# Optimization experiments

Hardware: AMD Instinct MI355X
Metric: run time of the kernel (lower is better)

Reference implementation:

```python
import jax, jax.numpy as jnp
import numpy as np

D_MODEL = 2048
N_HEADS = 16
KV_HEADS = 4
HEAD_DIM = D_MODEL // N_HEADS  # 128
GROUPS = N_HEADS // KV_HEADS   # 4
CLIP_QKV = 8.0
EPS = 1e-5
MAX_POS = 2048
ROPE_THETA = 10000.0


def _make_rope(max_pos, dim, theta):
    inv_freq = 1.0 / (theta ** (np.arange(0, dim, 2, dtype=np.float32) / dim))
    t = np.arange(max_pos, dtype=np.float32)
    freqs = np.outer(t, inv_freq)                      # [max_pos, dim/2]
    emb = np.concatenate([freqs, freqs], axis=-1)      # [max_pos, dim]
    return jnp.asarray(np.sin(emb)), jnp.asarray(np.cos(emb))


def setup_inputs() -> dict:
    key = jax.random.key(0)
    ks = jax.random.split(key, 6)
    B, S = 2, 2048
    hidden_states = jax.random.normal(ks[0], (B, S, D_MODEL), dtype=jnp.float32)
    attention_mask = jnp.ones((B, S), dtype=jnp.int32)
    position_ids = jnp.broadcast_to(jnp.arange(S, dtype=jnp.int32)[None, :], (B, S))
    init_std = 0.02
    qkv_out = D_MODEL + 2 * KV_HEADS * HEAD_DIM
    wqkv = jax.random.normal(ks[1], (D_MODEL, qkv_out), dtype=jnp.float32) * init_std
    w_out = jax.random.normal(ks[2], (D_MODEL, D_MODEL), dtype=jnp.float32) * init_std
    norm1_w = jnp.ones((D_MODEL,), dtype=jnp.float32)
    norm2_w = jnp.ones((D_MODEL,), dtype=jnp.float32)
    rope_sin, rope_cos = _make_rope(MAX_POS, HEAD_DIM, ROPE_THETA)
    return {
        'hidden_states': hidden_states,
        'attention_mask': attention_mask,
        'position_ids': position_ids,
        'wqkv': wqkv,
        'w_out': w_out,
        'norm1_w': norm1_w,
        'norm2_w': norm2_w,
        'rope_sin': rope_sin,
        'rope_cos': rope_cos,
    }


def _rmsnorm(x, w, eps=EPS):
    var = jnp.mean(jnp.square(x), axis=-1, keepdims=True)
    return (x * jax.lax.rsqrt(var + eps)) * w


def _rotate_half(x):
    h = x.shape[-1] // 2
    return jnp.concatenate([-x[..., h:], x[..., :h]], axis=-1)


def reference(hidden_states, attention_mask, position_ids, wqkv, w_out, norm1_w, norm2_w, rope_sin, rope_cos):
    B, S, _ = hidden_states.shape
    residual = hidden_states
    # pre-norm
    x = _rmsnorm(hidden_states, norm1_w)
    # fused QKV projection + clip
    qkv = jnp.clip(x @ wqkv, -CLIP_QKV, CLIP_QKV)
    q = qkv[..., :D_MODEL].reshape(B, S, N_HEADS, HEAD_DIM)
    kv_sz = KV_HEADS * HEAD_DIM
    k = qkv[..., D_MODEL:D_MODEL + kv_sz].reshape(B, S, KV_HEADS, HEAD_DIM)
    v = qkv[..., D_MODEL + kv_sz:].reshape(B, S, KV_HEADS, HEAD_DIM)
    # rotary embedding (bshd layout)
    sin = rope_sin[position_ids][:, :, None, :]  # [B,S,1,hd]
    cos = rope_cos[position_ids][:, :, None, :]
    q = q * cos + _rotate_half(q) * sin
    k = k * cos + _rotate_half(k) * sin
    # GQA head repeat
    k = jnp.repeat(k, GROUPS, axis=2)  # [B,S,H,hd]
    v = jnp.repeat(v, GROUPS, axis=2)
    # attention
    scale = 1.0 / jnp.sqrt(jnp.float32(HEAD_DIM))
    scores = jnp.einsum('bqhd,bkhd->bhqk', q, k) * scale
    causal = jnp.tril(jnp.ones((S, S), dtype=bool))
    mask = causal[None, None, :, :] & (attention_mask[:, None, None, :] > 0)
    scores = jnp.where(mask, scores, jnp.finfo(scores.dtype).min)
    probs = jax.nn.softmax(scores, axis=-1)
    attn = jnp.einsum('bhqk,bkhd->bqhd', probs, v).reshape(B, S, D_MODEL)
    attn = attn @ w_out
    # residual add (resid dropout deterministic -> identity) + post-norm
    hidden = residual + attn
    residual_out = hidden
    post = _rmsnorm(hidden, norm2_w)
    return residual_out, post
```

## Files before the change

kernel.cpp:

```cpp
#include <hip/hip_runtime.h>
#include <cstdint>
#include <cstddef>

#define D_MODEL 2048
#define SEQ     2048
#define NB      2
#define ROWS    4096
#define QKV_N   3072
#define NH      16
#define NKV     4
#define HD      128
#define EPSV    1e-5f
#define QPRE    (0.08838834764831845f * 1.4426950408889634f)

typedef unsigned short ushort_t;
typedef __attribute__((ext_vector_type(8))) short  short8;
typedef __attribute__((ext_vector_type(4))) short  short4v;
typedef __attribute__((ext_vector_type(4))) float  floatx4;

__device__ __forceinline__ ushort_t f2b(float f) {
    unsigned u = __float_as_uint(f);
    u += 0x7fffu + ((u >> 16) & 1u);
    return (ushort_t)(u >> 16);
}
__device__ __forceinline__ float b2f(ushort_t u) {
    return __uint_as_float(((unsigned)u) << 16);
}

__device__ __forceinline__ unsigned pkbf(float lo, float hi) {
    unsigned u0 = __float_as_uint(lo) + 0x8000u;
    unsigned u1 = __float_as_uint(hi) + 0x8000u;
    return __builtin_amdgcn_perm(u1, u0, 0x07060302u);
}

#if __has_builtin(__builtin_amdgcn_mfma_f32_16x16x16bf16_1k)
#define HAVE_1K 1
#endif

__device__ __forceinline__ floatx4 pv_mfma(short4v a, short4v b, floatx4 c) {
#ifdef HAVE_1K
    return __builtin_amdgcn_mfma_f32_16x16x16bf16_1k(a, b, c, 0, 0, 0);
#else
    short8 a8 = {a[0], a[1], a[2], a[3], 0, 0, 0, 0};
    short8 b8 = {b[0], b[1], b[2], b[3], 0, 0, 0, 0};
    return __builtin_amdgcn_mfma_f32_16x16x32_bf16(a8, b8, c, 0, 0, 0);
#endif
}

#define GLD_LDS16(gp, lp) __builtin_amdgcn_global_load_lds( \
    (const __attribute__((address_space(1))) void*)(gp),   \
    (__attribute__((address_space(3))) void*)(lp), 16, 0, 0)

__global__ __launch_bounds__(256) void k_rmsnorm_bf16(
        const float* __restrict__ x, const float* __restrict__ w,
        ushort_t* __restrict__ out) {
    int row = blockIdx.x, t = threadIdx.x;
    const float4* xr = (const float4*)(x + (size_t)row * D_MODEL);
    float4 a = xr[t], b = xr[t + 256];
    float ss = a.x*a.x + a.y*a.y + a.z*a.z + a.w*a.w
             + b.x*b.x + b.y*b.y + b.z*b.z + b.w*b.w;
    for (int m = 1; m < 64; m <<= 1) ss += __shfl_xor(ss, m);
    __shared__ float sred[4];
    if ((t & 63) == 0) sred[t >> 6] = ss;
    __syncthreads();
    float r = rsqrtf((sred[0] + sred[1] + sred[2] + sred[3]) * (1.0f / D_MODEL) + EPSV);
    const float4* wr = (const float4*)w;
    float4 wa = wr[t], wb = wr[t + 256];
    ushort4 pa, pb;
    pa.x = f2b(a.x * r * wa.x); pa.y = f2b(a.y * r * wa.y);
    pa.z = f2b(a.z * r * wa.z); pa.w = f2b(a.w * r * wa.w);
    pb.x = f2b(b.x * r * wb.x); pb.y = f2b(b.y * r * wb.y);
    pb.z = f2b(b.z * r * wb.z); pb.w = f2b(b.w * r * wb.w);
    ushort4* o = (ushort4*)(out + (size_t)row * D_MODEL);
    o[t] = pa; o[t + 256] = pb;
}

__global__ __launch_bounds__(256) void k_rmsnorm_f32(
        const float* __restrict__ x, const float* __restrict__ w,
        float* __restrict__ out) {
    int row = blockIdx.x, t = threadIdx.x;
    const float4* xr = (const float4*)(x + (size_t)row * D_MODEL);
    float4 a = xr[t], b = xr[t + 256];
    float ss = a.x*a.x + a.y*a.y + a.z*a.z + a.w*a.w
             + b.x*b.x + b.y*b.y + b.z*b.z + b.w*b.w;
    for (int m = 1; m < 64; m <<= 1) ss += __shfl_xor(ss, m);
    __shared__ float sred[4];
    if ((t & 63) == 0) sred[t >> 6] = ss;
    __syncthreads();
    float r = rsqrtf((sred[0] + sred[1] + sred[2] + sred[3]) * (1.0f / D_MODEL) + EPSV);
    const float4* wr = (const float4*)w;
    float4 wa = wr[t], wb = wr[t + 256];
    float4 oa, ob;
    oa.x = a.x * r * wa.x; oa.y = a.y * r * wa.y; oa.z = a.z * r * wa.z; oa.w = a.w * r * wa.w;
    ob.x = b.x * r * wb.x; ob.y = b.y * r * wb.y; ob.z = b.z * r * wb.z; ob.w = b.w * r * wb.w;
    float4* o = (float4*)(out + (size_t)row * D_MODEL);
    o[t] = oa; o[t + 256] = ob;
}

__global__ __launch_bounds__(256) void k_transpose_cvt(
        const float* __restrict__ in, ushort_t* __restrict__ out, int R, int C) {
    __shared__ float tile[32][33];
    int bc = blockIdx.x * 32, br = blockIdx.y * 32;
    int t = threadIdx.x, lr = t >> 5, lc = t & 31;
    for (int i = 0; i < 4; i++)
        tile[lr + i * 8][lc] = in[(size_t)(br + lr + i * 8) * C + bc + lc];
    __syncthreads();
    for (int i = 0; i < 4; i++)
        out[(size_t)(bc + lr + i * 8) * R + br + lc] = f2b(tile[lc][lr + i * 8]);
}

template <int MODE>
__global__ __launch_bounds__(256) void k_gemm(
        const ushort_t* __restrict__ A, const ushort_t* __restrict__ Bt,
        void* __restrict__ Cout, const float* __restrict__ resid,
        int M, int N, int K) {
    __shared__ __align__(16) ushort_t sA[128 * 32];
    __shared__ __align__(16) ushort_t sB[128 * 32];
    int bm = blockIdx.y * 128, bn = blockIdx.x * 128;
    int t = threadIdx.x;
    int wv = t >> 6, lane = t & 63;
    int wm = (wv >> 1) * 64, wn = (wv & 1) * 64;
    int q4 = lane >> 4, n16 = lane & 15;

    int srow = lane >> 2, scol = (lane & 3) * 8;
    const ushort_t* gA0 = A  + (size_t)(bm + wv * 32 + srow) * K + scol;
    const ushort_t* gA1 = gA0 + (size_t)16 * K;
    const ushort_t* gB0 = Bt + (size_t)(bn + wv * 32 + srow) * K + scol;
    const ushort_t* gB1 = gB0 + (size_t)16 * K;
    ushort_t* lA0 = sA + wv * 1024;
    ushort_t* lA1 = lA0 + 512;
    ushort_t* lB0 = sB + wv * 1024;
    ushort_t* lB1 = lB0 + 512;

    floatx4 zero4 = {0.0f, 0.0f, 0.0f, 0.0f};
    floatx4 acc[4][4];
    for (int i = 0; i < 4; i++)
        for (int j = 0; j < 4; j++) acc[i][j] = zero4;

    for (int k0 = 0; k0 < K; k0 += 32) {
        GLD_LDS16(gA0 + k0, lA0);
        GLD_LDS16(gA1 + k0, lA1);
        GLD_LDS16(gB0 + k0, lB0);
        GLD_LDS16(gB1 + k0, lB1);
        __syncthreads();
        short8 af[4], bfr[4];
        for (int i = 0; i < 4; i++) af[i]  = *(const short8*)&sA[(wm + i * 16 + n16) * 32 + q4 * 8];
        for (int j = 0; j < 4; j++) bfr[j] = *(const short8*)&sB[(wn + j * 16 + n16) * 32 + q4 * 8];
        for (int i = 0; i < 4; i++)
            for (int j = 0; j < 4; j++)
                acc[i][j] = __builtin_amdgcn_mfma_f32_16x16x32_bf16(af[i], bfr[j], acc[i][j], 0, 0, 0);
        __syncthreads();
    }

    for (int i = 0; i < 4; i++) {
        int rbase = bm + wm + i * 16 + q4 * 4;
        for (int j = 0; j < 4; j++) {
            int col = bn + wn + j * 16 + n16;
            if (MODE == 0) {
                ushort_t* C = (ushort_t*)Cout;
                for (int r = 0; r < 4; r++) {
                    float v = acc[i][j][r];
                    v = fminf(fmaxf(v, -8.0f), 8.0f);
                    C[(size_t)(rbase + r) * N + col] = f2b(v);
                }
            } else {
                float* C = (float*)Cout;
                for (int r = 0; r < 4; r++) {
                    float v = acc[i][j][r] + resid[(size_t)(rbase + r) * N + col];
                    C[(size_t)(rbase + r) * N + col] = v;
                }
            }
        }
    }
}

__global__ __launch_bounds__(256) void k_rope(
        const ushort_t* __restrict__ qkv, const int* __restrict__ pos_ids,
        const float* __restrict__ rsin, const float* __restrict__ rcos,
        ushort_t* __restrict__ qout, ushort_t* __restrict__ kout) {
    int wid  = blockIdx.x * 4 + (threadIdx.x >> 6);
    int lane = threadIdx.x & 63;
    int row = wid / 20, slot = wid - row * 20;
    int b = row >> 11, s = row & 2047;
    int pos = pos_ids[row];
    int col0 = (slot < 16) ? slot * HD : D_MODEL + (slot - 16) * HD;
    const ushort_t* src = qkv + (size_t)row * QKV_N + col0;
    float xl = b2f(src[lane]);
    float xh = b2f(src[lane + 64]);
    const float* cp = rcos + (size_t)pos * HD;
    const float* sp = rsin + (size_t)pos * HD;
    float cl = cp[lane], sl = sp[lane];
    float ch = cp[lane + 64], sh = sp[lane + 64];
    float mul = (slot < 16) ? QPRE : 1.0f;
    float ol = (xl * cl - xh * sl) * mul;
    float oh = (xh * ch + xl * sh) * mul;
    if (slot < 16) {
        size_t dst = ((size_t)(b * NH + slot) * SEQ + s) * HD;
        qout[dst + lane] = f2b(ol); qout[dst + lane + 64] = f2b(oh);
    } else {
        size_t dst = ((size_t)(b * NKV + (slot - 16)) * SEQ + s) * HD;
        kout[dst + lane] = f2b(ol); kout[dst + lane + 64] = f2b(oh);
    }
}

__global__ __launch_bounds__(256) void k_vtrans(
        const ushort_t* __restrict__ qkv, ushort_t* __restrict__ vt) {
    __shared__ ushort_t tile[32][33];
    int bh = blockIdx.z;
    int b = bh >> 2, h = bh & 3;
    int s0 = blockIdx.x * 32, d0 = blockIdx.y * 32;
    int t = threadIdx.x, lr = t >> 5, lc = t & 31;
    int col0 = D_MODEL + NKV * HD + h * HD;
    for (int i = 0; i < 4; i++)
        tile[lr + i * 8][lc] =
            qkv[((size_t)b * SEQ + s0 + lr + i * 8) * QKV_N + col0 + d0 + lc];
    __syncthreads();
    for (int i = 0; i < 4; i++)
        vt[((size_t)bh * HD + d0 + lr + i * 8) * SEQ + s0 + lc] = tile[lc][lr + i * 8];
}

__global__ __launch_bounds__(256, 4) void k_attn(
        const ushort_t* __restrict__ Q, const ushort_t* __restrict__ Kr,
        const ushort_t* __restrict__ Vt, const int* __restrict__ amask,
        ushort_t* __restrict__ O) {
    int bidx = blockIdx.x;
    int qt = (SEQ / 64 - 1) - (bidx >> 5);
    int bh = bidx & 31, h = bh & 15, b = bh >> 4;
    int wave = threadIdx.x >> 6, lane = threadIdx.x & 63;
    int q4 = lane >> 4, n16 = lane & 15;

    __shared__ __align__(16) ushort_t sK[64 * 128];
    __shared__ __align__(16) ushort_t sV[128 * 64];

    const ushort_t* Qh = Q  + (size_t)bh * SEQ * HD;
    const ushort_t* Kh = Kr + (size_t)(b * NKV + (h >> 2)) * SEQ * HD;
    const ushort_t* Vh = Vt + (size_t)(b * NKV + (h >> 2)) * HD * SEQ;
    const int* am = amask + b * SEQ;

    int q0 = qt * 64 + wave * 16;
    int qcol = q0 + n16;

    short8 qf[4];
    for (int kk = 0; kk < 4; kk++)
        qf[kk] = *(const short8*)(Qh + (size_t)qcol * HD + kk * 32 + q4 * 8);

    floatx4 zero4 = {0.0f, 0.0f, 0.0f, 0.0f};
    floatx4 o_acc[8];
    for (int dt = 0; dt < 8; dt++) o_acc[dt] = zero4;
    float m_i = -INFINITY, l_i = 0.0f;

    int krow_l = (lane >> 4);
    int kc_l   = lane & 15;
    int vrow_l = (lane >> 3);
    int vc_l   = lane & 7;

    int kv_iters = qt + 1;
    for (int it = 0; it < kv_iters; it++) {
        int kv0 = it * 64;
        __syncthreads();
        #pragma unroll
        for (int t = 0; t < 4; t++) {
            int krow = wave * 16 + t * 4 + krow_l;
            int kc   = kc_l ^ (krow & 7);
            GLD_LDS16(Kh + (size_t)(kv0 + krow) * HD + kc * 8,
                      sK + (wave * 16 + t * 4) * 128);
            int vrow = wave * 32 + t * 8 + vrow_l;
            int vc   = vc_l ^ (vrow & 7);
            GLD_LDS16(Vh + (size_t)vrow * SEQ + kv0 + vc * 8,
                      sV + (wave * 32 + t * 8) * 64);
        }
        __syncthreads();

        bool tail = (kv0 + 63 > q0);
        floatx4 st[4];
        for (int jj = 0; jj < 4; jj++) st[jj] = zero4;
        for (int jj = 0; jj < 4; jj++) {
            int krow = jj * 16 + n16;
            int sw = krow & 7;
            const ushort_t* kb = sK + krow * 128;
            for (int kk = 0; kk < 4; kk++) {
                short8 kf = *(const short8*)(kb + ((kk * 4 + q4) ^ sw) * 8);
                st[jj] = __builtin_amdgcn_mfma_f32_16x16x32_bf16(kf, qf[kk], st[jj], 0, 0, 0);
            }
        }
        for (int jj = 0; jj < 4; jj++) {
            int kvb = kv0 + jj * 16 + q4 * 4;
            int4 am4 = *(const int4*)(am + kvb);
            int amr[4] = {am4.x, am4.y, am4.z, am4.w};
            if (tail) {
                for (int r = 0; r < 4; r++)
                    st[jj][r] = (amr[r] > 0 && kvb + r <= qcol) ? st[jj][r] : -1e30f;
            } else {
                for (int r = 0; r < 4; r++)
                    st[jj][r] = (amr[r] > 0) ? st[jj][r] : -1e30f;
            }
        }
        float mx = st[0][0];
        for (int jj = 0; jj < 4; jj++)
            for (int r = 0; r < 4; r++) mx = fmaxf(mx, st[jj][r]);
        mx = fmaxf(mx, __shfl_xor(mx, 16));
        mx = fmaxf(mx, __shfl_xor(mx, 32));
        float mnew = fmaxf(m_i, mx);
        float al = exp2f(m_i - mnew);
        m_i = mnew;
        float rs = 0.0f;
        for (int jj = 0; jj < 4; jj++)
            for (int r = 0; r < 4; r++) {
                float p = exp2f(st[jj][r] - mnew);
                st[jj][r] = p;
                rs += p;
            }
        rs += __shfl_xor(rs, 16);
        rs += __shfl_xor(rs, 32);
        l_i = l_i * al + rs;
        for (int dt = 0; dt < 8; dt++)
            o_acc[dt] *= al;
        for (int jj = 0; jj < 4; jj++) {
            union { unsigned u[2]; short4v s; } uu;
            uu.u[0] = pkbf(st[jj][0], st[jj][1]);
            uu.u[1] = pkbf(st[jj][2], st[jj][3]);
            short4v pfr = uu.s;
            int ch = jj * 2 + (q4 >> 1), hh = q4 & 1;
            for (int dt = 0; dt < 8; dt++) {
                int vrow = dt * 16 + n16;
                short4v vf = *(const short4v*)(sV + vrow * 64 + ((ch ^ (vrow & 7)) * 8) + hh * 4);
                o_acc[dt] = pv_mfma(vf, pfr, o_acc[dt]);
            }
        }
    }
    float inv = 1.0f / l_i;
    ushort_t* orow = O + ((size_t)(b * SEQ) + qcol) * D_MODEL + h * HD + q4 * 4;
    for (int dt = 0; dt < 8; dt++) {
        uint2 pk;
        pk.x = pkbf(o_acc[dt][0] * inv, o_acc[dt][1] * inv);
        pk.y = pkbf(o_acc[dt][2] * inv, o_acc[dt][3] * inv);
        *(uint2*)(orow + dt * 16) = pk;
    }
}

extern "C" void kernel_launch(void* const* d_in, const int* in_sizes, int n_in,
                              void* d_out, int out_size, void* d_ws, size_t ws_size,
                              hipStream_t stream) {
    const float* hidden = (const float*)d_in[0];
    const int*   amask  = (const int*)d_in[1];
    const int*   pos    = (const int*)d_in[2];
    const float* wqkv   = (const float*)d_in[3];
    const float* wout   = (const float*)d_in[4];
    const float* n1w    = (const float*)d_in[5];
    const float* n2w    = (const float*)d_in[6];
    const float* rsin   = (const float*)d_in[7];
    const float* rcos   = (const float*)d_in[8];
    float* out0 = (float*)d_out;
    float* out1 = out0 + (size_t)ROWS * D_MODEL;

    char* ws = (char*)d_ws;
    ushort_t* x_bf    = (ushort_t*)ws;  ws += (size_t)ROWS * D_MODEL * 2;
    ushort_t* wqkv_t  = (ushort_t*)ws;  ws += (size_t)QKV_N * D_MODEL * 2;
    ushort_t* wout_t  = (ushort_t*)ws;  ws += (size_t)D_MODEL * D_MODEL * 2;
    ushort_t* qkv     = (ushort_t*)ws;  ws += (size_t)ROWS * QKV_N * 2;
    ushort_t* qrot    = (ushort_t*)ws;  ws += (size_t)NB * NH * SEQ * HD * 2;
    ushort_t* krot    = (ushort_t*)ws;  ws += (size_t)NB * NKV * SEQ * HD * 2;
    ushort_t* vt      = (ushort_t*)ws;  ws += (size_t)NB * NKV * HD * SEQ * 2;
    ushort_t* attn    = (ushort_t*)ws;  ws += (size_t)ROWS * D_MODEL * 2;

    k_rmsnorm_bf16<<<ROWS, 256, 0, stream>>>(hidden, n1w, x_bf);
    k_transpose_cvt<<<dim3(QKV_N / 32, D_MODEL / 32), 256, 0, stream>>>(wqkv, wqkv_t, D_MODEL, QKV_N);
    k_transpose_cvt<<<dim3(D_MODEL / 32, D_MODEL / 32), 256, 0, stream>>>(wout, wout_t, D_MODEL, D_MODEL);
    k_gemm<0><<<dim3(QKV_N / 128, ROWS / 128), 256, 0, stream>>>(x_bf, wqkv_t, qkv, nullptr, ROWS, QKV_N, D_MODEL);
    k_rope<<<ROWS * 20 / 4, 256, 0, stream>>>(qkv, pos, rsin, rcos, qrot, krot);
    k_vtrans<<<dim3(SEQ / 32, HD / 32, NB * NKV), 256, 0, stream>>>(qkv, vt);
    k_attn<<<(SEQ / 64) * 32, 256, 0, stream>>>(qrot, krot, vt, amask, attn);
    k_gemm<1><<<dim3(D_MODEL / 128, ROWS / 128), 256, 0, stream>>>(attn, wout_t, out0, hidden, ROWS, D_MODEL, D_MODEL);
    k_rmsnorm_f32<<<ROWS, 256, 0, stream>>>(out0, n2w, out1);
}
```

Before: 392.1 us.

## Double-buffer K/V tiles in attention and skip rescale when max grows little

Splits the K/V shared-memory staging into two buffers so the next tile's global-to-LDS load is issued while the current tile is computed, with one barrier per iteration in place of two. It also adds a lazy online-softmax rescale: the accumulator and running sum are rescaled only when the new row max exceeds the old one by more than 8 (log2 domain). Occupancy is lowered to 2 blocks per CU because LDS per block doubles. The lazy rescale lets exp2 arguments reach up to 2^8, which relies on fp32 headroom and bf16 packing of probabilities above 1.

```diff
diff --git a/kernel.cpp b/kernel.cpp
--- a/kernel.cpp
+++ b/kernel.cpp
@@ -219,7 +219,7 @@
         vt[((size_t)bh * HD + d0 + lr + i * 8) * SEQ + s0 + lc] = tile[lc][lr + i * 8];
 }
 
-__global__ __launch_bounds__(256, 4) void k_attn(
+__global__ __launch_bounds__(256, 2) void k_attn(
         const ushort_t* __restrict__ Q, const ushort_t* __restrict__ Kr,
         const ushort_t* __restrict__ Vt, const int* __restrict__ amask,
         ushort_t* __restrict__ O) {
@@ -229,8 +229,8 @@
     int wave = threadIdx.x >> 6, lane = threadIdx.x & 63;
     int q4 = lane >> 4, n16 = lane & 15;
 
-    __shared__ __align__(16) ushort_t sK[64 * 128];
-    __shared__ __align__(16) ushort_t sV[128 * 64];
+    __shared__ __align__(16) ushort_t sK[2][64 * 128];
+    __shared__ __align__(16) ushort_t sV[2][128 * 64];
 
     const ushort_t* Qh = Q  + (size_t)bh * SEQ * HD;
     const ushort_t* Kh = Kr + (size_t)(b * NKV + (h >> 2)) * SEQ * HD;
@@ -254,22 +254,35 @@
     int vrow_l = (lane >> 3);
     int vc_l   = lane & 7;
 
-    int kv_iters = qt + 1;
-    for (int it = 0; it < kv_iters; it++) {
-        int kv0 = it * 64;
-        __syncthreads();
+    auto stage_kv = [&](int buf, int kv0) {
         #pragma unroll
         for (int t = 0; t < 4; t++) {
             int krow = wave * 16 + t * 4 + krow_l;
             int kc   = kc_l ^ (krow & 7);
             GLD_LDS16(Kh + (size_t)(kv0 + krow) * HD + kc * 8,
-                      sK + (wave * 16 + t * 4) * 128);
+                      &sK[buf][(wave * 16 + t * 4) * 128]);
             int vrow = wave * 32 + t * 8 + vrow_l;
             int vc   = vc_l ^ (vrow & 7);
             GLD_LDS16(Vh + (size_t)vrow * SEQ + kv0 + vc * 8,
-                      sV + (wave * 32 + t * 8) * 64);
-        }
-        __syncthreads();
+                      &sV[buf][(wave * 32 + t * 8) * 64]);
+        }
+    };
+
+    int kv_iters = qt + 1;
+
+    stage_kv(0, 0);
+    asm volatile("s_waitcnt vmcnt(0)" ::: "memory");
+    __builtin_amdgcn_s_barrier();
+    __builtin_amdgcn_sched_barrier(0);
+
+    for (int it = 0; it < kv_iters; it++) {
+        int cur = it & 1;
+        int kv0 = it * 64;
+        if (it + 1 < kv_iters)
+            stage_kv(cur ^ 1, kv0 + 64);
+
+        const ushort_t* sKc = sK[cur];
+        const ushort_t* sVc = sV[cur];
 
         bool tail = (kv0 + 63 > q0);
         floatx4 st[4];
@@ -277,7 +290,7 @@
         for (int jj = 0; jj < 4; jj++) {
             int krow = jj * 16 + n16;
             int sw = krow & 7;
-            const ushort_t* kb = sK + krow * 128;
+            const ushort_t* kb = sKc + krow * 128;
             for (int kk = 0; kk < 4; kk++) {
                 short8 kf = *(const short8*)(kb + ((kk * 4 + q4) ^ sw) * 8);
                 st[jj] = __builtin_amdgcn_mfma_f32_16x16x32_bf16(kf, qf[kk], st[jj], 0, 0, 0);
@@ -300,21 +313,24 @@
             for (int r = 0; r < 4; r++) mx = fmaxf(mx, st[jj][r]);
         mx = fmaxf(mx, __shfl_xor(mx, 16));
         mx = fmaxf(mx, __shfl_xor(mx, 32));
-        float mnew = fmaxf(m_i, mx);
-        float al = exp2f(m_i - mnew);
-        m_i = mnew;
+        if (!__all(mx - m_i <= 8.0f)) {
+            float mnew = fmaxf(m_i, mx);
+            float al = exp2f(m_i - mnew);
+            m_i = mnew;
+            l_i *= al;
+            for (int dt = 0; dt < 8; dt++)
+                o_acc[dt] *= al;
+        }
         float rs = 0.0f;
         for (int jj = 0; jj < 4; jj++)
             for (int r = 0; r < 4; r++) {
-                float p = exp2f(st[jj][r] - mnew);
+                float p = exp2f(st[jj][r] - m_i);
                 st[jj][r] = p;
                 rs += p;
             }
         rs += __shfl_xor(rs, 16);
         rs += __shfl_xor(rs, 32);
-        l_i = l_i * al + rs;
-        for (int dt = 0; dt < 8; dt++)
-            o_acc[dt] *= al;
+        l_i += rs;
         for (int jj = 0; jj < 4; jj++) {
             union { unsigned u[2]; short4v s; } uu;
             uu.u[0] = pkbf(st[jj][0], st[jj][1]);
@@ -323,10 +339,13 @@
             int ch = jj * 2 + (q4 >> 1), hh = q4 & 1;
             for (int dt = 0; dt < 8; dt++) {
                 int vrow = dt * 16 + n16;
-                short4v vf = *(const short4v*)(sV + vrow * 64 + ((ch ^ (vrow & 7)) * 8) + hh * 4);
+                short4v vf = *(const short4v*)(sVc + vrow * 64 + ((ch ^ (vrow & 7)) * 8) + hh * 4);
                 o_acc[dt] = pv_mfma(vf, pfr, o_acc[dt]);
             }
         }
+        asm volatile("s_waitcnt vmcnt(0)" ::: "memory");
+        __builtin_amdgcn_s_barrier();
+        __builtin_amdgcn_sched_barrier(0);
     }
     float inv = 1.0f / l_i;
     ushort_t* orow = O + ((size_t)(b * SEQ) + qcol) * D_MODEL + h * HD + q4 * 4;
```

New measurement: 392.4 us. Within noise of the previous version (+0.1%).

## Process 128-row KV tiles per barrier with lazy softmax rescaling

Applied to the files above, without the earlier changes.

Doubles the KV tile loaded into shared memory to 128 rows and processes it as two 64-row halves, halving the number of barrier and load-issue rounds per query tile. Adds a lazy online-softmax rescale that skips updating the running max and accumulators unless the new max exceeds the old by more than a threshold. The larger shared memory footprint lowers the occupancy bound from 4 to 2 blocks per CU, which may reduce latency hiding.

```diff
diff --git a/kernel.cpp b/kernel.cpp
--- a/kernel.cpp
+++ b/kernel.cpp
@@ -219,7 +219,7 @@
         vt[((size_t)bh * HD + d0 + lr + i * 8) * SEQ + s0 + lc] = tile[lc][lr + i * 8];
 }
 
-__global__ __launch_bounds__(256, 4) void k_attn(
+__global__ __launch_bounds__(256, 2) void k_attn(
         const ushort_t* __restrict__ Q, const ushort_t* __restrict__ Kr,
         const ushort_t* __restrict__ Vt, const int* __restrict__ amask,
         ushort_t* __restrict__ O) {
@@ -229,8 +229,8 @@
     int wave = threadIdx.x >> 6, lane = threadIdx.x & 63;
     int q4 = lane >> 4, n16 = lane & 15;
 
-    __shared__ __align__(16) ushort_t sK[64 * 128];
-    __shared__ __align__(16) ushort_t sV[128 * 64];
+    __shared__ __align__(16) ushort_t sK[128 * 128];
+    __shared__ __align__(16) ushort_t sV[128 * 128];
 
     const ushort_t* Qh = Q  + (size_t)bh * SEQ * HD;
     const ushort_t* Kh = Kr + (size_t)(b * NKV + (h >> 2)) * SEQ * HD;
@@ -249,82 +249,92 @@
     for (int dt = 0; dt < 8; dt++) o_acc[dt] = zero4;
     float m_i = -INFINITY, l_i = 0.0f;
 
-    int krow_l = (lane >> 4);
-    int kc_l   = lane & 15;
-    int vrow_l = (lane >> 3);
-    int vc_l   = lane & 7;
-
-    int kv_iters = qt + 1;
+    int row_l = lane >> 4;
+    int c16   = lane & 15;
+
+    int kv_iters = (qt >> 1) + 1;
+
     for (int it = 0; it < kv_iters; it++) {
-        int kv0 = it * 64;
+        int kv0 = it * 128;
         __syncthreads();
         #pragma unroll
-        for (int t = 0; t < 4; t++) {
-            int krow = wave * 16 + t * 4 + krow_l;
-            int kc   = kc_l ^ (krow & 7);
+        for (int t = 0; t < 8; t++) {
+            int krow = wave * 32 + t * 4 + row_l;
+            int kc   = c16 ^ (krow & 7);
             GLD_LDS16(Kh + (size_t)(kv0 + krow) * HD + kc * 8,
-                      sK + (wave * 16 + t * 4) * 128);
-            int vrow = wave * 32 + t * 8 + vrow_l;
-            int vc   = vc_l ^ (vrow & 7);
+                      sK + (wave * 32 + t * 4) * 128);
+            int vrow = wave * 32 + t * 4 + row_l;
+            int vc   = (c16 & 8) | ((c16 & 7) ^ (vrow & 7));
             GLD_LDS16(Vh + (size_t)vrow * SEQ + kv0 + vc * 8,
-                      sV + (wave * 32 + t * 8) * 64);
+                      sV + (wave * 32 + t * 4) * 128);
         }
-        __syncthreads();
-
-        bool tail = (kv0 + 63 > q0);
-        floatx4 st[4];
-        for (int jj = 0; jj < 4; jj++) st[jj] = zero4;
-        for (int jj = 0; jj < 4; jj++) {
-            int krow = jj * 16 + n16;
-            int sw = krow & 7;
-            const ushort_t* kb = sK + krow * 128;
-            for (int kk = 0; kk < 4; kk++) {
-                short8 kf = *(const short8*)(kb + ((kk * 4 + q4) ^ sw) * 8);
-                st[jj] = __builtin_amdgcn_mfma_f32_16x16x32_bf16(kf, qf[kk], st[jj], 0, 0, 0);
-            }
-        }
-        for (int jj = 0; jj < 4; jj++) {
-            int kvb = kv0 + jj * 16 + q4 * 4;
-            int4 am4 = *(const int4*)(am + kvb);
-            int amr[4] = {am4.x, am4.y, am4.z, am4.w};
-            if (tail) {
-                for (int r = 0; r < 4; r++)
-                    st[jj][r] = (amr[r] > 0 && kvb + r <= qcol) ? st[jj][r] : -1e30f;
-            } else {
-                for (int r = 0; r < 4; r++)
-                    st[jj][r] = (amr[r] > 0) ? st[jj][r] : -1e30f;
-            }
-        }
-        float mx = st[0][0];
-        for (int jj = 0; jj < 4; jj++)
-            for (int r = 0; r < 4; r++) mx = fmaxf(mx, st[jj][r]);
-        mx = fmaxf(mx, __shfl_xor(mx, 16));
-        mx = fmaxf(mx, __shfl_xor(mx, 32));
-        float mnew = fmaxf(m_i, mx);
-        float al = exp2f(m_i - mnew);
-        m_i = mnew;
-        float rs = 0.0f;
-        for (int jj = 0; jj < 4; jj++)
-            for (int r = 0; r < 4; r++) {
-                float p = exp2f(st[jj][r] - mnew);
-                st[jj][r] = p;
-                rs += p;
-            }
-        rs += __shfl_xor(rs, 16);
-        rs += __shfl_xor(rs, 32);
-        l_i = l_i * al + rs;
-        for (int dt = 0; dt < 8; dt++)
-            o_acc[dt] *= al;
-        for (int jj = 0; jj < 4; jj++) {
-            union { unsigned u[2]; short4v s; } uu;
-            uu.u[0] = pkbf(st[jj][0], st[jj][1]);
-            uu.u[1] = pkbf(st[jj][2], st[jj][3]);
-            short4v pfr = uu.s;
-            int ch = jj * 2 + (q4 >> 1), hh = q4 & 1;
-            for (int dt = 0; dt < 8; dt++) {
-                int vrow = dt * 16 + n16;
-                short4v vf = *(const short4v*)(sV + vrow * 64 + ((ch ^ (vrow & 7)) * 8) + hh * 4);
-                o_acc[dt] = pv_mfma(vf, pfr, o_acc[dt]);
+        asm volatile("s_waitcnt vmcnt(0)" ::: "memory");
+        __builtin_amdgcn_s_barrier();
+        __builtin_amdgcn_sched_barrier(0);
+
+        #pragma unroll
+        for (int hb = 0; hb < 2; hb++) {
+            int kvbase = kv0 + hb * 64;
+            if (kvbase > qt * 64 + 63) break;
+            bool tail = (kvbase + 63 > q0);
+            floatx4 st[4];
+            for (int jj = 0; jj < 4; jj++) st[jj] = zero4;
+            for (int jj = 0; jj < 4; jj++) {
+                int krow = hb * 64 + jj * 16 + n16;
+                int sw = krow & 7;
+                const ushort_t* kb = sK + krow * 128;
+                for (int kk = 0; kk < 4; kk++) {
+                    short8 kf = *(const short8*)(kb + ((kk * 4 + q4) ^ sw) * 8);
+                    st[jj] = __builtin_amdgcn_mfma_f32_16x16x32_bf16(kf, qf[kk], st[jj], 0, 0, 0);
+                }
+            }
+            for (int jj = 0; jj < 4; jj++) {
+                int kvb = kvbase + jj * 16 + q4 * 4;
+                int4 am4 = *(const int4*)(am + kvb);
+                int amr[4] = {am4.x, am4.y, am4.z, am4.w};
+                if (tail) {
+                    for (int r = 0; r < 4; r++)
+                        st[jj][r] = (amr[r] > 0 && kvb + r <= qcol) ? st[jj][r] : -1e30f;
+                } else {
+                    for (int r = 0; r < 4; r++)
+                        st[jj][r] = (amr[r] > 0) ? st[jj][r] : -1e30f;
+                }
+            }
+            float mx = st[0][0];
+            for (int jj = 0; jj < 4; jj++)
+                for (int r = 0; r < 4; r++) mx = fmaxf(mx, st[jj][r]);
+            mx = fmaxf(mx, __shfl_xor(mx, 16));
+            mx = fmaxf(mx, __shfl_xor(mx, 32));
+            if (!__all(mx - m_i <= 8.0f)) {
+                float mnew = fmaxf(m_i, mx);
+                float al = exp2f(m_i - mnew);
+                m_i = mnew;
+                l_i *= al;
+                for (int dt = 0; dt < 8; dt++)
+                    o_acc[dt] *= al;
+            }
+            float rs = 0.0f;
+            for (int jj = 0; jj < 4; jj++)
+                for (int r = 0; r < 4; r++) {
+                    float p = exp2f(st[jj][r] - m_i);
+                    st[jj][r] = p;
+                    rs += p;
+                }
+            rs += __shfl_xor(rs, 16);
+            rs += __shfl_xor(rs, 32);
+            l_i += rs;
+            for (int jj = 0; jj < 4; jj++) {
+                union { unsigned u[2]; short4v s; } uu;
+                uu.u[0] = pkbf(st[jj][0], st[jj][1]);
+                uu.u[1] = pkbf(st[jj][2], st[jj][3]);
+                short4v pfr = uu.s;
+                int ch = jj * 2 + (q4 >> 1), hh = q4 & 1;
+                for (int dt = 0; dt < 8; dt++) {
+                    int vrow = dt * 16 + n16;
+                    short4v vf = *(const short4v*)(sV + vrow * 128 + hb * 64 +
+                                                   ((ch ^ (vrow & 7)) * 8) + hh * 4);
+                    o_acc[dt] = pv_mfma(vf, pfr, o_acc[dt]);
+                }
             }
         }
     }
```

Result: no change. 390.1 us (-0.5%).
